# Performance work log

Measured on AMD Instinct MI355X. Metric: run time of the kernel, lower is better.

The kernel has to match this reference:

```python
import jax, jax.numpy as jnp
import numpy as np

RBF_DIM = 16
RBF_DMAX = 10.0
EPS = 1e-8


def _rbf(d):
    # GVP-style radial basis featurization: [..., RBF_DIM]
    mu = jnp.linspace(0.0, RBF_DMAX, RBF_DIM)
    sigma = RBF_DMAX / RBF_DIM
    return jnp.exp(-(((d[..., None] - mu) / sigma) ** 2))


def _norm_no_nan(x):
    return jnp.sqrt(jnp.clip(jnp.sum(x * x, axis=-1), EPS, None))


def setup_inputs() -> dict:
    key = jax.random.key(0)
    ks = jax.random.split(key, 16)
    N, Eu = 100000, 800000
    D_node, D_edge = 128, 64
    n_a, n_e = 16, 5
    s_t = jax.random.normal(ks[0], (N, D_node), jnp.float32)
    x_t = jax.random.normal(ks[1], (N, 3), jnp.float32) * 3.0
    v_t = jax.random.normal(ks[2], (N, 4, 3), jnp.float32)
    e_t = jax.random.normal(ks[3], (2 * Eu, D_edge), jnp.float32)
    dst_lig_x = x_t + jax.random.normal(ks[4], (N, 3), jnp.float32)
    dst_lig_a = jax.random.uniform(ks[5], (N, n_a), jnp.float32)
    dst_lig_e = jax.random.uniform(ks[6], (Eu, n_e), jnp.float32)
    # symmetric edge list: first Eu edges are "upper", second Eu their mirror
    src_u = jax.random.randint(ks[7], (Eu,), 0, N)
    dst_u = jax.random.randint(ks[8], (Eu,), 0, N)
    edge_src = jnp.concatenate([src_u, dst_u]).astype(jnp.int64)
    edge_dst = jnp.concatenate([dst_u, src_u]).astype(jnp.int64)
    # node residual MLP params (in = rbf + one-hot lig_a + s_t)
    din_n = RBF_DIM + n_a + D_node
    W1 = jax.random.normal(ks[9], (din_n, D_node), jnp.float32) / np.sqrt(din_n)
    b1 = jnp.zeros((D_node,), jnp.float32)
    W2 = jax.random.normal(ks[10], (D_node, D_node), jnp.float32) / np.sqrt(D_node)
    b2 = jnp.zeros((D_node,), jnp.float32)
    # edge residual MLP params (in = e_t + lig_e pred + rbf)
    din_e = D_edge + n_e + RBF_DIM
    We = jax.random.normal(ks[11], (din_e, D_edge), jnp.float32) / np.sqrt(din_e)
    be = jnp.zeros((D_edge,), jnp.float32)
    return {"s_t": s_t, "x_t": x_t, "v_t": v_t, "e_t": e_t,
            "dst_lig_x": dst_lig_x, "dst_lig_a": dst_lig_a, "dst_lig_e": dst_lig_e,
            "edge_src": edge_src, "edge_dst": edge_dst,
            "W1": W1, "b1": b1, "W2": W2, "b2": b2, "We": We, "be": be}


def reference(s_t, x_t, v_t, e_t, dst_lig_x, dst_lig_a, dst_lig_e,
              edge_src, edge_dst, W1, b1, W2, b2, We, be):
    # ---- node residual (lig_x generated -> RBF of |x_pred - x_t|; lig_a generated -> pred) ----
    x_diff = dst_lig_x - x_t                      # [N,3]
    dij = _norm_no_nan(x_diff)                    # [N]
    node_in = jnp.concatenate([_rbf(dij), dst_lig_a, s_t], axis=-1)
    h = jax.nn.silu(node_in @ W1 + b1)
    node_res = jax.nn.silu(h @ W2 + b2)
    node_out = s_t + node_res
    # overwrite last vector channel with unit displacement
    v_out = v_t.at[:, -1, :].set(x_diff / dij[:, None])
    # ---- lig_to_lig edge residual on upper edges, mirrored to lower edges ----
    Eu = edge_src.shape[0] // 2
    su, du = edge_src[:Eu], edge_dst[:Eu]
    d_t = _norm_no_nan(x_t[su] - x_t[du])         # current distances
    d_1 = _norm_no_nan(dst_lig_x[su] - dst_lig_x[du])  # predicted distances
    d_input = _rbf(d_1) - _rbf(d_t)               # [Eu, RBF_DIM]
    e_u = e_t[:Eu]
    edge_in = jnp.concatenate([e_u, dst_lig_e, d_input], axis=-1)
    edge_res = jax.nn.silu(edge_in @ We + be)
    feats = e_u + edge_res
    # original scatters feats into both upper-mask and ~upper-mask slots
    e_out = jnp.concatenate([feats, feats], axis=0)
    return node_out, v_out, e_out
```

## Files before the change

### kernel.cpp

```cpp
#include <hip/hip_runtime.h>
#include <math.h>

typedef short bf16x8 __attribute__((ext_vector_type(8)));
typedef float f32x4 __attribute__((ext_vector_type(4)));
typedef float fvec4 __attribute__((ext_vector_type(4)));

#define EBK 128
#define NBK 64

__device__ __forceinline__ float silu_f(float x) {
  return x / (1.0f + __expf(-x));
}
__device__ __forceinline__ unsigned short f2bf(float x) {
  union { float f; unsigned u; } v; v.f = x;
  unsigned r = v.u + 0x7FFFu + ((v.u >> 16) & 1u);
  return (unsigned short)(r >> 16);
}
__device__ __forceinline__ float bf2f(unsigned short h) {
  union { unsigned u; float f; } v; v.u = ((unsigned)h) << 16; return v.f;
}

__global__ __launch_bounds__(256)
void prep_kernel(const float* __restrict__ W1, const float* __restrict__ W2,
                 const float* __restrict__ We, unsigned short* __restrict__ ws)
{
  int i = blockIdx.x * 256 + threadIdx.x;
  if (i < 6144) {
    int col = i / 96, k = i - col * 96;
    float v = (k < 85) ? We[k * 64 + col] : 0.0f;
    ws[i] = f2bf(v);
  }
  int j = i - 6144;
  if (j >= 0 && j < 20480) {
    int col = j / 160, k = j - col * 160;
    ws[6144 + j] = f2bf(W1[k * 128 + col]);
  }
  int l = i - 26624;
  if (l >= 0 && l < 16384) {
    int col = l >> 7, k = l & 127;
    ws[26624 + l] = f2bf(W2[k * 128 + col]);
  }
}

__global__ __launch_bounds__(256, 4)
void node_kernel(const float* __restrict__ s_t,
                 const float* __restrict__ x_t,
                 const float* __restrict__ v_t,
                 const float* __restrict__ dst_lig_x,
                 const float* __restrict__ dst_lig_a,
                 const unsigned short* __restrict__ w1t, const float* __restrict__ b1,
                 const unsigned short* __restrict__ w2t, const float* __restrict__ b2,
                 float* __restrict__ node_out, float* __restrict__ v_out,
                 int N)
{
  __shared__ unsigned short A1[NBK][168];
  __shared__ unsigned short H [NBK][136];
  const int t = threadIdx.x;
  const int row0 = blockIdx.x * NBK;
  const int w = t >> 6, lane = t & 63;

  #pragma unroll
  for (int p = 0; p < 8; ++p) {
    int i = p * 256 + t;
    int row = i >> 5, q = i & 31;
    if (row0 + row < N) {
      const fvec4 v = __builtin_nontemporal_load(
          reinterpret_cast<const fvec4*>(&s_t[(size_t)(row0 + row) * 128 + q * 4]));
      uint2 pk;
      pk.x = f2bf(v.x) | ((unsigned)f2bf(v.y) << 16);
      pk.y = f2bf(v.z) | ((unsigned)f2bf(v.w) << 16);
      *reinterpret_cast<uint2*>(&A1[row][32 + q * 4]) = pk;
    }
  }
  #pragma unroll
  for (int p = 0; p < 4; ++p) {
    int i = p * 256 + t;
    int el = i >> 4, m = i & 15;
    int row = row0 + el;
    if (row < N) {
      float dx = dst_lig_x[row*3+0] - x_t[row*3+0];
      float dy = dst_lig_x[row*3+1] - x_t[row*3+1];
      float dz = dst_lig_x[row*3+2] - x_t[row*3+2];
      float dij = sqrtf(fmaxf(dx*dx + dy*dy + dz*dz, 1e-8f));
      float tt = (dij - 0.66666667f * (float)m) * 1.6f;
      A1[el][m]      = f2bf(__expf(-tt * tt));
      A1[el][16 + m] = f2bf(dst_lig_a[(size_t)row * 16 + m]);
      if (m < 12) {
        float val;
        if (m < 9)       val = v_t[(size_t)row * 12 + m];
        else if (m == 9) val = dx / dij;
        else if (m == 10)val = dy / dij;
        else             val = dz / dij;
        __builtin_nontemporal_store(val, &v_out[(size_t)row * 12 + m]);
      }
    }
  }
  __syncthreads();

  const int mb = (w & 1) * 32;
  const int nb = (w >> 1) * 64;

  f32x4 acc[2][4] = {};
  #pragma unroll 1
  for (int ks = 0; ks < 5; ++ks) {
    const int ko = ks * 32 + ((lane >> 4) << 3);
    bf16x8 af[2], bfr[4];
    #pragma unroll
    for (int m = 0; m < 2; ++m)
      af[m] = *reinterpret_cast<const bf16x8*>(&A1[mb + m*16 + (lane & 15)][ko]);
    #pragma unroll
    for (int n = 0; n < 4; ++n)
      bfr[n] = *reinterpret_cast<const bf16x8*>(&w1t[(size_t)(nb + n*16 + (lane & 15)) * 160 + ko]);
    #pragma unroll
    for (int m = 0; m < 2; ++m)
      #pragma unroll
      for (int n = 0; n < 4; ++n)
        acc[m][n] = __builtin_amdgcn_mfma_f32_16x16x32_bf16(af[m], bfr[n], acc[m][n], 0, 0, 0);
  }
  #pragma unroll
  for (int n = 0; n < 4; ++n) {
    float bb = b1[nb + n*16 + (lane & 15)];
    #pragma unroll
    for (int m = 0; m < 2; ++m) {
      int r0 = mb + m*16 + ((lane >> 4) << 2);
      int c  = nb + n*16 + (lane & 15);
      #pragma unroll
      for (int r = 0; r < 4; ++r)
        H[r0 + r][c] = f2bf(silu_f(acc[m][n][r] + bb));
    }
  }
  __syncthreads();

  f32x4 acc2[2][4] = {};
  #pragma unroll 1
  for (int ks = 0; ks < 4; ++ks) {
    const int ko = ks * 32 + ((lane >> 4) << 3);
    bf16x8 af[2], bfr[4];
    #pragma unroll
    for (int m = 0; m < 2; ++m)
      af[m] = *reinterpret_cast<const bf16x8*>(&H[mb + m*16 + (lane & 15)][ko]);
    #pragma unroll
    for (int n = 0; n < 4; ++n)
      bfr[n] = *reinterpret_cast<const bf16x8*>(&w2t[(size_t)(nb + n*16 + (lane & 15)) * 128 + ko]);
    #pragma unroll
    for (int m = 0; m < 2; ++m)
      #pragma unroll
      for (int n = 0; n < 4; ++n)
        acc2[m][n] = __builtin_amdgcn_mfma_f32_16x16x32_bf16(af[m], bfr[n], acc2[m][n], 0, 0, 0);
  }
  #pragma unroll
  for (int n = 0; n < 4; ++n) {
    float bb = b2[nb + n*16 + (lane & 15)];
    #pragma unroll
    for (int m = 0; m < 2; ++m) {
      int r0 = mb + m*16 + ((lane >> 4) << 2);
      int c  = nb + n*16 + (lane & 15);
      #pragma unroll
      for (int r = 0; r < 4; ++r) {
        int row = row0 + r0 + r;
        if (row < N) {
          float o = bf2f(A1[r0 + r][32 + c]) + silu_f(acc2[m][n][r] + bb);
          __builtin_nontemporal_store(o, &node_out[(size_t)row * 128 + c]);
        }
      }
    }
  }
}

__global__ __launch_bounds__(256, 6)
void edge_kernel(const float* __restrict__ e_t,
                 const float* __restrict__ x_t,
                 const float* __restrict__ dst_lig_x,
                 const float* __restrict__ dst_lig_e,
                 const int* __restrict__ edge_src,
                 const int* __restrict__ edge_dst,
                 const unsigned short* __restrict__ wet, const float* __restrict__ be,
                 float* __restrict__ e_out0, float* __restrict__ e_out1,
                 int Eu)
{
  __shared__ unsigned short T[EBK][36];
  const int t = threadIdx.x;
  const int e0 = blockIdx.x * EBK;
  const int w = t >> 6, lane = t & 63;

  {
    const int el = t >> 1, which = t & 1;
    const int e = e0 + el;
    float dcur = 0.0f;
    if (e < Eu) {
      int su = edge_src[e], du = edge_dst[e];
      const float* base = which ? dst_lig_x : x_t;
      float u0 = base[su*3+0] - base[du*3+0];
      float u1 = base[su*3+1] - base[du*3+1];
      float u2 = base[su*3+2] - base[du*3+2];
      dcur = sqrtf(fmaxf(u0*u0 + u1*u1 + u2*u2, 1e-8f));
    }
    float doth = __shfl_xor(dcur, 1);
    float dt_ = which ? doth : dcur;
    float d1_ = which ? dcur : doth;
    if (e < Eu) {
      #pragma unroll
      for (int q = 0; q < 8; ++q) {
        int m = which * 8 + q;
        float mu = 0.66666667f * (float)m;
        float a1 = (d1_ - mu) * 1.6f, a2 = (dt_ - mu) * 1.6f;
        T[el][5 + m] = f2bf(__expf(-a1*a1) - __expf(-a2*a2));
      }
    }
  }
  #pragma unroll
  for (int q = 0; q < 3; ++q) {
    int i = q * 256 + t;
    if (i < EBK * 5) {
      int el = i / 5, c = i - el * 5;
      if (e0 + el < Eu) T[el][c] = f2bf(dst_lig_e[(size_t)(e0 + el) * 5 + c]);
    }
  }
  #pragma unroll
  for (int q = 0; q < 6; ++q) {
    int i = q * 256 + t;
    if (i < EBK * 11) { int el = i / 11, c = i - el * 11; T[el][21 + c] = 0; }
  }
  __syncthreads();

  const int mb = w * 32;
  const int lr = lane & 15;
  const int koff = (lane >> 4) << 3;

  f32x4 acc[2][4] = {};
  #pragma unroll 1
  for (int ks = 0; ks < 2; ++ks) {
    bf16x8 af[2], bfr[4];
    #pragma unroll
    for (int m = 0; m < 2; ++m) {
      int row = e0 + mb + m*16 + lr;
      if (row >= Eu) row = Eu - 1;
      const float* ap = &e_t[(size_t)row * 64 + ks * 32 + koff];
      const fvec4 lo = *reinterpret_cast<const fvec4*>(ap);
      const fvec4 hi = *reinterpret_cast<const fvec4*>(ap + 4);
      union { bf16x8 v; unsigned u[4]; } pk;
      pk.u[0] = f2bf(lo.x) | ((unsigned)f2bf(lo.y) << 16);
      pk.u[1] = f2bf(lo.z) | ((unsigned)f2bf(lo.w) << 16);
      pk.u[2] = f2bf(hi.x) | ((unsigned)f2bf(hi.y) << 16);
      pk.u[3] = f2bf(hi.z) | ((unsigned)f2bf(hi.w) << 16);
      af[m] = pk.v;
    }
    #pragma unroll
    for (int n = 0; n < 4; ++n)
      bfr[n] = *reinterpret_cast<const bf16x8*>(&wet[(size_t)(n*16 + lr) * 96 + ks * 32 + koff]);
    #pragma unroll
    for (int m = 0; m < 2; ++m)
      #pragma unroll
      for (int n = 0; n < 4; ++n)
        acc[m][n] = __builtin_amdgcn_mfma_f32_16x16x32_bf16(af[m], bfr[n], acc[m][n], 0, 0, 0);
  }
  {
    bf16x8 af[2], bfr[4];
    #pragma unroll
    for (int m = 0; m < 2; ++m)
      af[m] = *reinterpret_cast<const bf16x8*>(&T[mb + m*16 + lr][koff]);
    #pragma unroll
    for (int n = 0; n < 4; ++n)
      bfr[n] = *reinterpret_cast<const bf16x8*>(&wet[(size_t)(n*16 + lr) * 96 + 64 + koff]);
    #pragma unroll
    for (int m = 0; m < 2; ++m)
      #pragma unroll
      for (int n = 0; n < 4; ++n)
        acc[m][n] = __builtin_amdgcn_mfma_f32_16x16x32_bf16(af[m], bfr[n], acc[m][n], 0, 0, 0);
  }

  #pragma unroll
  for (int n = 0; n < 4; ++n) {
    float bb = be[n*16 + lr];
    #pragma unroll
    for (int m = 0; m < 2; ++m) {
      int r0 = mb + m*16 + ((lane >> 4) << 2);
      int c  = n*16 + lr;
      #pragma unroll
      for (int r = 0; r < 4; ++r) {
        size_t eidx = (size_t)e0 + r0 + r;
        if ((int)eidx < Eu) {
          float feat = e_t[eidx * 64 + c] + silu_f(acc[m][n][r] + bb);
          __builtin_nontemporal_store(feat, &e_out0[eidx * 64 + c]);
          __builtin_nontemporal_store(feat, &e_out1[eidx * 64 + c]);
        }
      }
    }
  }
}

extern "C" void kernel_launch(void* const* d_in, const int* in_sizes, int n_in,
                              void* d_out, int out_size, void* d_ws, size_t ws_size,
                              hipStream_t stream) {
  const float* s_t       = (const float*)d_in[0];
  const float* x_t       = (const float*)d_in[1];
  const float* v_t       = (const float*)d_in[2];
  const float* e_t       = (const float*)d_in[3];
  const float* dst_lig_x = (const float*)d_in[4];
  const float* dst_lig_a = (const float*)d_in[5];
  const float* dst_lig_e = (const float*)d_in[6];
  const int*   edge_src  = (const int*)d_in[7];
  const int*   edge_dst  = (const int*)d_in[8];
  const float* W1        = (const float*)d_in[9];
  const float* b1        = (const float*)d_in[10];
  const float* W2        = (const float*)d_in[11];
  const float* b2        = (const float*)d_in[12];
  const float* We        = (const float*)d_in[13];
  const float* be        = (const float*)d_in[14];

  const int N  = in_sizes[0] / 128;
  const int Eu = in_sizes[3] / 128;

  float* out      = (float*)d_out;
  float* node_out = out;
  float* v_out    = out + (size_t)N * 128;
  float* e_out0   = v_out + (size_t)N * 12;
  float* e_out1   = e_out0 + (size_t)Eu * 64;

  unsigned short* wsp = (unsigned short*)d_ws;
  unsigned short* wet = wsp;
  unsigned short* w1t = wsp + 6144;
  unsigned short* w2t = wsp + 26624;

  prep_kernel<<<168, 256, 0, stream>>>(W1, W2, We, wsp);

  edge_kernel<<<(Eu + EBK - 1) / EBK, 256, 0, stream>>>(
      e_t, x_t, dst_lig_x, dst_lig_e, edge_src, edge_dst, wet, be,
      e_out0, e_out1, Eu);

  node_kernel<<<(N + NBK - 1) / NBK, 256, 0, stream>>>(
      s_t, x_t, v_t, dst_lig_x, dst_lig_a, w1t, b1, w2t, b2,
      node_out, v_out, N);
}
```

Before: 246.9 us.

## Use 512-thread edge blocks with early e_t loads and one M-tile per wave

The edge kernel now launches 512 threads per block, so each of 8 waves handles one 16-row M tile instead of two. The e_t A-fragment loads are issued before the RBF/LDS staging phase so their latency overlaps that work. The residual e_t reads are also batched into registers ahead of the epilogue, and the fp32-to-bf16 conversion becomes truncation instead of round-to-nearest-even. Truncation slightly changes numerical accuracy, and launch_bounds(512,6) may constrain registers.

```diff
diff --git a/kernel.cpp b/kernel.cpp
--- a/kernel.cpp
+++ b/kernel.cpp
@@ -18,6 +18,10 @@
 }
 __device__ __forceinline__ float bf2f(unsigned short h) {
   union { unsigned u; float f; } v; v.u = ((unsigned)h) << 16; return v.f;
+}
+__device__ __forceinline__ unsigned pack_trunc(float lo, float hi) {
+  union { float f; unsigned u; } a, b; a.f = lo; b.f = hi;
+  return (b.u & 0xFFFF0000u) | (a.u >> 16);
 }
 
 __global__ __launch_bounds__(256)
@@ -167,7 +171,7 @@
   }
 }
 
-__global__ __launch_bounds__(256, 6)
+__global__ __launch_bounds__(512, 6)
 void edge_kernel(const float* __restrict__ e_t,
                  const float* __restrict__ x_t,
                  const float* __restrict__ dst_lig_x,
@@ -182,8 +186,20 @@
   const int t = threadIdx.x;
   const int e0 = blockIdx.x * EBK;
   const int w = t >> 6, lane = t & 63;
-
-  {
+  const int lr = lane & 15;
+  const int koff = (lane >> 4) << 3;
+  const int mb = w * 16;
+
+  int arow = e0 + mb + lr;
+  if (arow >= Eu) arow = Eu - 1;
+  const fvec4* ap = reinterpret_cast<const fvec4*>(&e_t[(size_t)arow * 64]);
+  const int fi = koff >> 2;
+  fvec4 a00 = ap[fi];
+  fvec4 a01 = ap[fi + 1];
+  fvec4 a10 = ap[8 + fi];
+  fvec4 a11 = ap[8 + fi + 1];
+
+  if (t < 256) {
     const int el = t >> 1, which = t & 1;
     const int e = e0 + el;
     float dcur = 0.0f;
@@ -209,81 +225,81 @@
     }
   }
   #pragma unroll
-  for (int q = 0; q < 3; ++q) {
-    int i = q * 256 + t;
+  for (int q = 0; q < 2; ++q) {
+    int i = q * 512 + t;
     if (i < EBK * 5) {
       int el = i / 5, c = i - el * 5;
       if (e0 + el < Eu) T[el][c] = f2bf(dst_lig_e[(size_t)(e0 + el) * 5 + c]);
     }
   }
   #pragma unroll
-  for (int q = 0; q < 6; ++q) {
-    int i = q * 256 + t;
+  for (int q = 0; q < 3; ++q) {
+    int i = q * 512 + t;
     if (i < EBK * 11) { int el = i / 11, c = i - el * 11; T[el][21 + c] = 0; }
   }
   __syncthreads();
 
-  const int mb = w * 32;
-  const int lr = lane & 15;
-  const int koff = (lane >> 4) << 3;
-
-  f32x4 acc[2][4] = {};
-  #pragma unroll 1
-  for (int ks = 0; ks < 2; ++ks) {
-    bf16x8 af[2], bfr[4];
-    #pragma unroll
-    for (int m = 0; m < 2; ++m) {
-      int row = e0 + mb + m*16 + lr;
-      if (row >= Eu) row = Eu - 1;
-      const float* ap = &e_t[(size_t)row * 64 + ks * 32 + koff];
-      const fvec4 lo = *reinterpret_cast<const fvec4*>(ap);
-      const fvec4 hi = *reinterpret_cast<const fvec4*>(ap + 4);
-      union { bf16x8 v; unsigned u[4]; } pk;
-      pk.u[0] = f2bf(lo.x) | ((unsigned)f2bf(lo.y) << 16);
-      pk.u[1] = f2bf(lo.z) | ((unsigned)f2bf(lo.w) << 16);
-      pk.u[2] = f2bf(hi.x) | ((unsigned)f2bf(hi.y) << 16);
-      pk.u[3] = f2bf(hi.z) | ((unsigned)f2bf(hi.w) << 16);
-      af[m] = pk.v;
-    }
-    #pragma unroll
-    for (int n = 0; n < 4; ++n)
-      bfr[n] = *reinterpret_cast<const bf16x8*>(&wet[(size_t)(n*16 + lr) * 96 + ks * 32 + koff]);
-    #pragma unroll
-    for (int m = 0; m < 2; ++m)
-      #pragma unroll
-      for (int n = 0; n < 4; ++n)
-        acc[m][n] = __builtin_amdgcn_mfma_f32_16x16x32_bf16(af[m], bfr[n], acc[m][n], 0, 0, 0);
-  }
+  union { bf16x8 v; unsigned u[4]; } af0, af1, af2;
+  af0.u[0] = pack_trunc(a00.x, a00.y);
+  af0.u[1] = pack_trunc(a00.z, a00.w);
+  af0.u[2] = pack_trunc(a01.x, a01.y);
+  af0.u[3] = pack_trunc(a01.z, a01.w);
+  af1.u[0] = pack_trunc(a10.x, a10.y);
+  af1.u[1] = pack_trunc(a10.z, a10.w);
+  af1.u[2] = pack_trunc(a11.x, a11.y);
+  af1.u[3] = pack_trunc(a11.z, a11.w);
+  af2.v = *reinterpret_cast<const bf16x8*>(&T[mb + lr][koff]);
+
+  f32x4 acc[4] = {};
   {
-    bf16x8 af[2], bfr[4];
-    #pragma unroll
-    for (int m = 0; m < 2; ++m)
-      af[m] = *reinterpret_cast<const bf16x8*>(&T[mb + m*16 + lr][koff]);
-    #pragma unroll
-    for (int n = 0; n < 4; ++n)
-      bfr[n] = *reinterpret_cast<const bf16x8*>(&wet[(size_t)(n*16 + lr) * 96 + 64 + koff]);
-    #pragma unroll
-    for (int m = 0; m < 2; ++m)
-      #pragma unroll
-      for (int n = 0; n < 4; ++n)
-        acc[m][n] = __builtin_amdgcn_mfma_f32_16x16x32_bf16(af[m], bfr[n], acc[m][n], 0, 0, 0);
-  }
-
+    bf16x8 b0, b1_, b2_, b3;
+    b0 = *reinterpret_cast<const bf16x8*>(&wet[(size_t)(0*16 + lr) * 96 + 0*32 + koff]);
+    b1_= *reinterpret_cast<const bf16x8*>(&wet[(size_t)(1*16 + lr) * 96 + 0*32 + koff]);
+    b2_= *reinterpret_cast<const bf16x8*>(&wet[(size_t)(2*16 + lr) * 96 + 0*32 + koff]);
+    b3 = *reinterpret_cast<const bf16x8*>(&wet[(size_t)(3*16 + lr) * 96 + 0*32 + koff]);
+    acc[0] = __builtin_amdgcn_mfma_f32_16x16x32_bf16(af0.v, b0, acc[0], 0, 0, 0);
+    acc[1] = __builtin_amdgcn_mfma_f32_16x16x32_bf16(af0.v, b1_, acc[1], 0, 0, 0);
+    acc[2] = __builtin_amdgcn_mfma_f32_16x16x32_bf16(af0.v, b2_, acc[2], 0, 0, 0);
+    acc[3] = __builtin_amdgcn_mfma_f32_16x16x32_bf16(af0.v, b3, acc[3], 0, 0, 0);
+    b0 = *reinterpret_cast<const bf16x8*>(&wet[(size_t)(0*16 + lr) * 96 + 1*32 + koff]);
+    b1_= *reinterpret_cast<const bf16x8*>(&wet[(size_t)(1*16 + lr) * 96 + 1*32 + koff]);
+    b2_= *reinterpret_cast<const bf16x8*>(&wet[(size_t)(2*16 + lr) * 96 + 1*32 + koff]);
+    b3 = *reinterpret_cast<const bf16x8*>(&wet[(size_t)(3*16 + lr) * 96 + 1*32 + koff]);
+    acc[0] = __builtin_amdgcn_mfma_f32_16x16x32_bf16(af1.v, b0, acc[0], 0, 0, 0);
+    acc[1] = __builtin_amdgcn_mfma_f32_16x16x32_bf16(af1.v, b1_, acc[1], 0, 0, 0);
+    acc[2] = __builtin_amdgcn_mfma_f32_16x16x32_bf16(af1.v, b2_, acc[2], 0, 0, 0);
+    acc[3] = __builtin_amdgcn_mfma_f32_16x16x32_bf16(af1.v, b3, acc[3], 0, 0, 0);
+    b0 = *reinterpret_cast<const bf16x8*>(&wet[(size_t)(0*16 + lr) * 96 + 64 + koff]);
+    b1_= *reinterpret_cast<const bf16x8*>(&wet[(size_t)(1*16 + lr) * 96 + 64 + koff]);
+    b2_= *reinterpret_cast<const bf16x8*>(&wet[(size_t)(2*16 + lr) * 96 + 64 + koff]);
+    b3 = *reinterpret_cast<const bf16x8*>(&wet[(size_t)(3*16 + lr) * 96 + 64 + koff]);
+    acc[0] = __builtin_amdgcn_mfma_f32_16x16x32_bf16(af2.v, b0, acc[0], 0, 0, 0);
+    acc[1] = __builtin_amdgcn_mfma_f32_16x16x32_bf16(af2.v, b1_, acc[1], 0, 0, 0);
+    acc[2] = __builtin_amdgcn_mfma_f32_16x16x32_bf16(af2.v, b2_, acc[2], 0, 0, 0);
+    acc[3] = __builtin_amdgcn_mfma_f32_16x16x32_bf16(af2.v, b3, acc[3], 0, 0, 0);
+  }
+
+  const int r0 = mb + ((lane >> 4) << 2);
+  float res[4][4];
+  #pragma unroll
+  for (int n = 0; n < 4; ++n)
+    #pragma unroll
+    for (int r = 0; r < 4; ++r) {
+      size_t eidx = (size_t)e0 + r0 + r;
+      if ((int)eidx >= Eu) eidx = Eu - 1;
+      res[n][r] = e_t[eidx * 64 + n*16 + lr];
+    }
   #pragma unroll
   for (int n = 0; n < 4; ++n) {
     float bb = be[n*16 + lr];
-    #pragma unroll
-    for (int m = 0; m < 2; ++m) {
-      int r0 = mb + m*16 + ((lane >> 4) << 2);
-      int c  = n*16 + lr;
-      #pragma unroll
-      for (int r = 0; r < 4; ++r) {
-        size_t eidx = (size_t)e0 + r0 + r;
-        if ((int)eidx < Eu) {
-          float feat = e_t[eidx * 64 + c] + silu_f(acc[m][n][r] + bb);
-          __builtin_nontemporal_store(feat, &e_out0[eidx * 64 + c]);
-          __builtin_nontemporal_store(feat, &e_out1[eidx * 64 + c]);
-        }
+    int c = n*16 + lr;
+    #pragma unroll
+    for (int r = 0; r < 4; ++r) {
+      size_t eidx = (size_t)e0 + r0 + r;
+      if ((int)eidx < Eu) {
+        float feat = res[n][r] + silu_f(acc[n][r] + bb);
+        __builtin_nontemporal_store(feat, &e_out0[eidx * 64 + c]);
+        __builtin_nontemporal_store(feat, &e_out1[eidx * 64 + c]);
       }
     }
   }
@@ -324,7 +340,7 @@
 
   prep_kernel<<<168, 256, 0, stream>>>(W1, W2, We, wsp);
 
-  edge_kernel<<<(Eu + EBK - 1) / EBK, 256, 0, stream>>>(
+  edge_kernel<<<(Eu + EBK - 1) / EBK, 512, 0, stream>>>(
       e_t, x_t, dst_lig_x, dst_lig_e, edge_src, edge_dst, wet, be,
       e_out0, e_out1, Eu);
 
```

Result: slower. 262.0 us (+6.1%).

## Fuse node and edge kernels into one interleaved launch with shared LDS union

Applied to the files above, without the earlier changes.

Merges the separate edge and node kernels into one launch in which every fifth block does node work and the rest do edge work, so the two kinds of blocks overlap on the device instead of running back to back. Node and edge tiles share LDS through a union, and the hidden-layer buffer H now reuses the A1 space, with an extra barrier added to make that safe. The node residual now rereads s_t from global memory instead of the bf16 copy in LDS, which also changes rounding of the residual. The risks are that node blocks now run under the edge kernel's launch bounds (fewer registers), and that the branch makes the block mix uneven.

```diff
diff --git a/kernel.cpp b/kernel.cpp
--- a/kernel.cpp
+++ b/kernel.cpp
@@ -42,247 +42,257 @@
   }
 }
 
-__global__ __launch_bounds__(256, 4)
-void node_kernel(const float* __restrict__ s_t,
-                 const float* __restrict__ x_t,
-                 const float* __restrict__ v_t,
-                 const float* __restrict__ dst_lig_x,
-                 const float* __restrict__ dst_lig_a,
-                 const unsigned short* __restrict__ w1t, const float* __restrict__ b1,
-                 const unsigned short* __restrict__ w2t, const float* __restrict__ b2,
-                 float* __restrict__ node_out, float* __restrict__ v_out,
-                 int N)
+struct NodeSmem { unsigned short A1[NBK][168]; };
+struct EdgeSmem { unsigned short T[EBK][36]; };
+union FusedSmem { NodeSmem n; EdgeSmem e; };
+
+__global__ __launch_bounds__(256, 6)
+void fused_kernel(const float* __restrict__ s_t,
+                  const float* __restrict__ x_t,
+                  const float* __restrict__ v_t,
+                  const float* __restrict__ e_t,
+                  const float* __restrict__ dst_lig_x,
+                  const float* __restrict__ dst_lig_a,
+                  const float* __restrict__ dst_lig_e,
+                  const int* __restrict__ edge_src,
+                  const int* __restrict__ edge_dst,
+                  const unsigned short* __restrict__ wsw,
+                  const float* __restrict__ b1, const float* __restrict__ b2,
+                  const float* __restrict__ be,
+                  float* __restrict__ node_out, float* __restrict__ v_out,
+                  float* __restrict__ e_out0, float* __restrict__ e_out1,
+                  int N, int Eu, int nNodeBlk, int nEdgeBlk)
 {
-  __shared__ unsigned short A1[NBK][168];
-  __shared__ unsigned short H [NBK][136];
+  __shared__ FusedSmem sm;
+  const int bid = blockIdx.x;
   const int t = threadIdx.x;
-  const int row0 = blockIdx.x * NBK;
   const int w = t >> 6, lane = t & 63;
-
-  #pragma unroll
-  for (int p = 0; p < 8; ++p) {
-    int i = p * 256 + t;
-    int row = i >> 5, q = i & 31;
-    if (row0 + row < N) {
-      const fvec4 v = __builtin_nontemporal_load(
-          reinterpret_cast<const fvec4*>(&s_t[(size_t)(row0 + row) * 128 + q * 4]));
-      uint2 pk;
-      pk.x = f2bf(v.x) | ((unsigned)f2bf(v.y) << 16);
-      pk.y = f2bf(v.z) | ((unsigned)f2bf(v.w) << 16);
-      *reinterpret_cast<uint2*>(&A1[row][32 + q * 4]) = pk;
-    }
-  }
-  #pragma unroll
-  for (int p = 0; p < 4; ++p) {
-    int i = p * 256 + t;
-    int el = i >> 4, m = i & 15;
-    int row = row0 + el;
-    if (row < N) {
-      float dx = dst_lig_x[row*3+0] - x_t[row*3+0];
-      float dy = dst_lig_x[row*3+1] - x_t[row*3+1];
-      float dz = dst_lig_x[row*3+2] - x_t[row*3+2];
-      float dij = sqrtf(fmaxf(dx*dx + dy*dy + dz*dz, 1e-8f));
-      float tt = (dij - 0.66666667f * (float)m) * 1.6f;
-      A1[el][m]      = f2bf(__expf(-tt * tt));
-      A1[el][16 + m] = f2bf(dst_lig_a[(size_t)row * 16 + m]);
-      if (m < 12) {
-        float val;
-        if (m < 9)       val = v_t[(size_t)row * 12 + m];
-        else if (m == 9) val = dx / dij;
-        else if (m == 10)val = dy / dij;
-        else             val = dz / dij;
-        __builtin_nontemporal_store(val, &v_out[(size_t)row * 12 + m]);
-      }
-    }
-  }
-  __syncthreads();
-
-  const int mb = (w & 1) * 32;
-  const int nb = (w >> 1) * 64;
-
-  f32x4 acc[2][4] = {};
-  #pragma unroll 1
-  for (int ks = 0; ks < 5; ++ks) {
-    const int ko = ks * 32 + ((lane >> 4) << 3);
-    bf16x8 af[2], bfr[4];
-    #pragma unroll
-    for (int m = 0; m < 2; ++m)
-      af[m] = *reinterpret_cast<const bf16x8*>(&A1[mb + m*16 + (lane & 15)][ko]);
-    #pragma unroll
-    for (int n = 0; n < 4; ++n)
-      bfr[n] = *reinterpret_cast<const bf16x8*>(&w1t[(size_t)(nb + n*16 + (lane & 15)) * 160 + ko]);
-    #pragma unroll
-    for (int m = 0; m < 2; ++m)
-      #pragma unroll
-      for (int n = 0; n < 4; ++n)
-        acc[m][n] = __builtin_amdgcn_mfma_f32_16x16x32_bf16(af[m], bfr[n], acc[m][n], 0, 0, 0);
-  }
-  #pragma unroll
-  for (int n = 0; n < 4; ++n) {
-    float bb = b1[nb + n*16 + (lane & 15)];
-    #pragma unroll
-    for (int m = 0; m < 2; ++m) {
-      int r0 = mb + m*16 + ((lane >> 4) << 2);
-      int c  = nb + n*16 + (lane & 15);
-      #pragma unroll
-      for (int r = 0; r < 4; ++r)
-        H[r0 + r][c] = f2bf(silu_f(acc[m][n][r] + bb));
-    }
-  }
-  __syncthreads();
-
-  f32x4 acc2[2][4] = {};
-  #pragma unroll 1
-  for (int ks = 0; ks < 4; ++ks) {
-    const int ko = ks * 32 + ((lane >> 4) << 3);
-    bf16x8 af[2], bfr[4];
-    #pragma unroll
-    for (int m = 0; m < 2; ++m)
-      af[m] = *reinterpret_cast<const bf16x8*>(&H[mb + m*16 + (lane & 15)][ko]);
-    #pragma unroll
-    for (int n = 0; n < 4; ++n)
-      bfr[n] = *reinterpret_cast<const bf16x8*>(&w2t[(size_t)(nb + n*16 + (lane & 15)) * 128 + ko]);
-    #pragma unroll
-    for (int m = 0; m < 2; ++m)
-      #pragma unroll
-      for (int n = 0; n < 4; ++n)
-        acc2[m][n] = __builtin_amdgcn_mfma_f32_16x16x32_bf16(af[m], bfr[n], acc2[m][n], 0, 0, 0);
-  }
-  #pragma unroll
-  for (int n = 0; n < 4; ++n) {
-    float bb = b2[nb + n*16 + (lane & 15)];
-    #pragma unroll
-    for (int m = 0; m < 2; ++m) {
-      int r0 = mb + m*16 + ((lane >> 4) << 2);
-      int c  = nb + n*16 + (lane & 15);
-      #pragma unroll
-      for (int r = 0; r < 4; ++r) {
-        int row = row0 + r0 + r;
-        if (row < N) {
-          float o = bf2f(A1[r0 + r][32 + c]) + silu_f(acc2[m][n][r] + bb);
-          __builtin_nontemporal_store(o, &node_out[(size_t)row * 128 + c]);
-        }
-      }
-    }
-  }
-}
-
-__global__ __launch_bounds__(256, 6)
-void edge_kernel(const float* __restrict__ e_t,
-                 const float* __restrict__ x_t,
-                 const float* __restrict__ dst_lig_x,
-                 const float* __restrict__ dst_lig_e,
-                 const int* __restrict__ edge_src,
-                 const int* __restrict__ edge_dst,
-                 const unsigned short* __restrict__ wet, const float* __restrict__ be,
-                 float* __restrict__ e_out0, float* __restrict__ e_out1,
-                 int Eu)
-{
-  __shared__ unsigned short T[EBK][36];
-  const int t = threadIdx.x;
-  const int e0 = blockIdx.x * EBK;
-  const int w = t >> 6, lane = t & 63;
-
-  {
-    const int el = t >> 1, which = t & 1;
-    const int e = e0 + el;
-    float dcur = 0.0f;
-    if (e < Eu) {
-      int su = edge_src[e], du = edge_dst[e];
-      const float* base = which ? dst_lig_x : x_t;
-      float u0 = base[su*3+0] - base[du*3+0];
-      float u1 = base[su*3+1] - base[du*3+1];
-      float u2 = base[su*3+2] - base[du*3+2];
-      dcur = sqrtf(fmaxf(u0*u0 + u1*u1 + u2*u2, 1e-8f));
-    }
-    float doth = __shfl_xor(dcur, 1);
-    float dt_ = which ? doth : dcur;
-    float d1_ = which ? dcur : doth;
-    if (e < Eu) {
-      #pragma unroll
-      for (int q = 0; q < 8; ++q) {
-        int m = which * 8 + q;
-        float mu = 0.66666667f * (float)m;
-        float a1 = (d1_ - mu) * 1.6f, a2 = (dt_ - mu) * 1.6f;
-        T[el][5 + m] = f2bf(__expf(-a1*a1) - __expf(-a2*a2));
-      }
-    }
-  }
-  #pragma unroll
-  for (int q = 0; q < 3; ++q) {
-    int i = q * 256 + t;
-    if (i < EBK * 5) {
-      int el = i / 5, c = i - el * 5;
-      if (e0 + el < Eu) T[el][c] = f2bf(dst_lig_e[(size_t)(e0 + el) * 5 + c]);
-    }
-  }
-  #pragma unroll
-  for (int q = 0; q < 6; ++q) {
-    int i = q * 256 + t;
-    if (i < EBK * 11) { int el = i / 11, c = i - el * 11; T[el][21 + c] = 0; }
-  }
-  __syncthreads();
-
-  const int mb = w * 32;
   const int lr = lane & 15;
   const int koff = (lane >> 4) << 3;
 
-  f32x4 acc[2][4] = {};
-  #pragma unroll 1
-  for (int ks = 0; ks < 2; ++ks) {
-    bf16x8 af[2], bfr[4];
-    #pragma unroll
-    for (int m = 0; m < 2; ++m) {
-      int row = e0 + mb + m*16 + lr;
-      if (row >= Eu) row = Eu - 1;
-      const float* ap = &e_t[(size_t)row * 64 + ks * 32 + koff];
-      const fvec4 lo = *reinterpret_cast<const fvec4*>(ap);
-      const fvec4 hi = *reinterpret_cast<const fvec4*>(ap + 4);
-      union { bf16x8 v; unsigned u[4]; } pk;
-      pk.u[0] = f2bf(lo.x) | ((unsigned)f2bf(lo.y) << 16);
-      pk.u[1] = f2bf(lo.z) | ((unsigned)f2bf(lo.w) << 16);
-      pk.u[2] = f2bf(hi.x) | ((unsigned)f2bf(hi.y) << 16);
-      pk.u[3] = f2bf(hi.z) | ((unsigned)f2bf(hi.w) << 16);
-      af[m] = pk.v;
-    }
-    #pragma unroll
-    for (int n = 0; n < 4; ++n)
-      bfr[n] = *reinterpret_cast<const bf16x8*>(&wet[(size_t)(n*16 + lr) * 96 + ks * 32 + koff]);
-    #pragma unroll
-    for (int m = 0; m < 2; ++m)
+  if (bid % 5 == 4) {
+    const int nb = bid / 5;
+    if (nb >= nNodeBlk) return;
+    const int row0 = nb * NBK;
+    const unsigned short* w1t = wsw + 6144;
+    const unsigned short* w2t = wsw + 26624;
+    auto& A1 = sm.n.A1;
+    unsigned short* Hp = &sm.n.A1[0][0];
+
+    #pragma unroll
+    for (int p = 0; p < 8; ++p) {
+      int i = p * 256 + t;
+      int row = i >> 5, q = i & 31;
+      if (row0 + row < N) {
+        const fvec4 v = __builtin_nontemporal_load(
+            reinterpret_cast<const fvec4*>(&s_t[(size_t)(row0 + row) * 128 + q * 4]));
+        uint2 pk;
+        pk.x = f2bf(v.x) | ((unsigned)f2bf(v.y) << 16);
+        pk.y = f2bf(v.z) | ((unsigned)f2bf(v.w) << 16);
+        *reinterpret_cast<uint2*>(&A1[row][32 + q * 4]) = pk;
+      }
+    }
+    #pragma unroll
+    for (int p = 0; p < 4; ++p) {
+      int i = p * 256 + t;
+      int el = i >> 4, m = i & 15;
+      int row = row0 + el;
+      if (row < N) {
+        float dx = dst_lig_x[row*3+0] - x_t[row*3+0];
+        float dy = dst_lig_x[row*3+1] - x_t[row*3+1];
+        float dz = dst_lig_x[row*3+2] - x_t[row*3+2];
+        float dij = sqrtf(fmaxf(dx*dx + dy*dy + dz*dz, 1e-8f));
+        float tt = (dij - 0.66666667f * (float)m) * 1.6f;
+        A1[el][m]      = f2bf(__expf(-tt * tt));
+        A1[el][16 + m] = f2bf(dst_lig_a[(size_t)row * 16 + m]);
+        if (m < 12) {
+          float val;
+          if (m < 9)       val = v_t[(size_t)row * 12 + m];
+          else if (m == 9) val = dx / dij;
+          else if (m == 10)val = dy / dij;
+          else             val = dz / dij;
+          __builtin_nontemporal_store(val, &v_out[(size_t)row * 12 + m]);
+        }
+      }
+    }
+    __syncthreads();
+
+    const int mb = (w & 1) * 32;
+    const int nb2 = (w >> 1) * 64;
+
+    f32x4 acc[2][4] = {};
+    #pragma unroll 1
+    for (int ks = 0; ks < 5; ++ks) {
+      const int ko = ks * 32 + koff;
+      bf16x8 af[2], bfr[4];
+      #pragma unroll
+      for (int m = 0; m < 2; ++m)
+        af[m] = *reinterpret_cast<const bf16x8*>(&A1[mb + m*16 + lr][ko]);
       #pragma unroll
       for (int n = 0; n < 4; ++n)
-        acc[m][n] = __builtin_amdgcn_mfma_f32_16x16x32_bf16(af[m], bfr[n], acc[m][n], 0, 0, 0);
-  }
-  {
-    bf16x8 af[2], bfr[4];
-    #pragma unroll
-    for (int m = 0; m < 2; ++m)
-      af[m] = *reinterpret_cast<const bf16x8*>(&T[mb + m*16 + lr][koff]);
-    #pragma unroll
-    for (int n = 0; n < 4; ++n)
-      bfr[n] = *reinterpret_cast<const bf16x8*>(&wet[(size_t)(n*16 + lr) * 96 + 64 + koff]);
-    #pragma unroll
-    for (int m = 0; m < 2; ++m)
+        bfr[n] = *reinterpret_cast<const bf16x8*>(&w1t[(size_t)(nb2 + n*16 + lr) * 160 + ko]);
+      #pragma unroll
+      for (int m = 0; m < 2; ++m)
+        #pragma unroll
+        for (int n = 0; n < 4; ++n)
+          acc[m][n] = __builtin_amdgcn_mfma_f32_16x16x32_bf16(af[m], bfr[n], acc[m][n], 0, 0, 0);
+    }
+    __syncthreads();
+
+    #pragma unroll
+    for (int n = 0; n < 4; ++n) {
+      float bb = b1[nb2 + n*16 + lr];
+      #pragma unroll
+      for (int m = 0; m < 2; ++m) {
+        int r0 = mb + m*16 + ((lane >> 4) << 2);
+        int c  = nb2 + n*16 + lr;
+        #pragma unroll
+        for (int r = 0; r < 4; ++r)
+          Hp[(size_t)(r0 + r) * 136 + c] = f2bf(silu_f(acc[m][n][r] + bb));
+      }
+    }
+    __syncthreads();
+
+    f32x4 acc2[2][4] = {};
+    #pragma unroll 1
+    for (int ks = 0; ks < 4; ++ks) {
+      const int ko = ks * 32 + koff;
+      bf16x8 af[2], bfr[4];
+      #pragma unroll
+      for (int m = 0; m < 2; ++m)
+        af[m] = *reinterpret_cast<const bf16x8*>(&Hp[(size_t)(mb + m*16 + lr) * 136 + ko]);
       #pragma unroll
       for (int n = 0; n < 4; ++n)
-        acc[m][n] = __builtin_amdgcn_mfma_f32_16x16x32_bf16(af[m], bfr[n], acc[m][n], 0, 0, 0);
-  }
-
-  #pragma unroll
-  for (int n = 0; n < 4; ++n) {
-    float bb = be[n*16 + lr];
-    #pragma unroll
-    for (int m = 0; m < 2; ++m) {
-      int r0 = mb + m*16 + ((lane >> 4) << 2);
-      int c  = n*16 + lr;
-      #pragma unroll
-      for (int r = 0; r < 4; ++r) {
-        size_t eidx = (size_t)e0 + r0 + r;
-        if ((int)eidx < Eu) {
-          float feat = e_t[eidx * 64 + c] + silu_f(acc[m][n][r] + bb);
-          __builtin_nontemporal_store(feat, &e_out0[eidx * 64 + c]);
-          __builtin_nontemporal_store(feat, &e_out1[eidx * 64 + c]);
+        bfr[n] = *reinterpret_cast<const bf16x8*>(&w2t[(size_t)(nb2 + n*16 + lr) * 128 + ko]);
+      #pragma unroll
+      for (int m = 0; m < 2; ++m)
+        #pragma unroll
+        for (int n = 0; n < 4; ++n)
+          acc2[m][n] = __builtin_amdgcn_mfma_f32_16x16x32_bf16(af[m], bfr[n], acc2[m][n], 0, 0, 0);
+    }
+    #pragma unroll
+    for (int n = 0; n < 4; ++n) {
+      float bb = b2[nb2 + n*16 + lr];
+      #pragma unroll
+      for (int m = 0; m < 2; ++m) {
+        int r0 = mb + m*16 + ((lane >> 4) << 2);
+        int c  = nb2 + n*16 + lr;
+        #pragma unroll
+        for (int r = 0; r < 4; ++r) {
+          int row = row0 + r0 + r;
+          if (row < N) {
+            float o = s_t[(size_t)row * 128 + c] + silu_f(acc2[m][n][r] + bb);
+            __builtin_nontemporal_store(o, &node_out[(size_t)row * 128 + c]);
+          }
+        }
+      }
+    }
+  } else {
+    const int eb = bid - (bid + 1) / 5;
+    if (eb >= nEdgeBlk) return;
+    const int e0 = eb * EBK;
+    const unsigned short* wet = wsw;
+    auto& T = sm.e.T;
+
+    {
+      const int el = t >> 1, which = t & 1;
+      const int e = e0 + el;
+      float dcur = 0.0f;
+      if (e < Eu) {
+        int su = edge_src[e], du = edge_dst[e];
+        const float* base = which ? dst_lig_x : x_t;
+        float u0 = base[su*3+0] - base[du*3+0];
+        float u1 = base[su*3+1] - base[du*3+1];
+        float u2 = base[su*3+2] - base[du*3+2];
+        dcur = sqrtf(fmaxf(u0*u0 + u1*u1 + u2*u2, 1e-8f));
+      }
+      float doth = __shfl_xor(dcur, 1);
+      float dt_ = which ? doth : dcur;
+      float d1_ = which ? dcur : doth;
+      if (e < Eu) {
+        #pragma unroll
+        for (int q = 0; q < 8; ++q) {
+          int m = which * 8 + q;
+          float mu = 0.66666667f * (float)m;
+          float a1 = (d1_ - mu) * 1.6f, a2 = (dt_ - mu) * 1.6f;
+          T[el][5 + m] = f2bf(__expf(-a1*a1) - __expf(-a2*a2));
+        }
+      }
+    }
+    #pragma unroll
+    for (int q = 0; q < 3; ++q) {
+      int i = q * 256 + t;
+      if (i < EBK * 5) {
+        int el = i / 5, c = i - el * 5;
+        if (e0 + el < Eu) T[el][c] = f2bf(dst_lig_e[(size_t)(e0 + el) * 5 + c]);
+      }
+    }
+    #pragma unroll
+    for (int q = 0; q < 6; ++q) {
+      int i = q * 256 + t;
+      if (i < EBK * 11) { int el = i / 11, c = i - el * 11; T[el][21 + c] = 0; }
+    }
+    __syncthreads();
+
+    const int mb = w * 32;
+
+    f32x4 acc[2][4] = {};
+    #pragma unroll 1
+    for (int ks = 0; ks < 2; ++ks) {
+      bf16x8 af[2], bfr[4];
+      #pragma unroll
+      for (int m = 0; m < 2; ++m) {
+        int row = e0 + mb + m*16 + lr;
+        if (row >= Eu) row = Eu - 1;
+        const float* ap = &e_t[(size_t)row * 64 + ks * 32 + koff];
+        const fvec4 lo = *reinterpret_cast<const fvec4*>(ap);
+        const fvec4 hi = *reinterpret_cast<const fvec4*>(ap + 4);
+        union { bf16x8 v; unsigned u[4]; } pk;
+        pk.u[0] = f2bf(lo.x) | ((unsigned)f2bf(lo.y) << 16);
+        pk.u[1] = f2bf(lo.z) | ((unsigned)f2bf(lo.w) << 16);
+        pk.u[2] = f2bf(hi.x) | ((unsigned)f2bf(hi.y) << 16);
+        pk.u[3] = f2bf(hi.z) | ((unsigned)f2bf(hi.w) << 16);
+        af[m] = pk.v;
+      }
+      #pragma unroll
+      for (int n = 0; n < 4; ++n)
+        bfr[n] = *reinterpret_cast<const bf16x8*>(&wet[(size_t)(n*16 + lr) * 96 + ks * 32 + koff]);
+      #pragma unroll
+      for (int m = 0; m < 2; ++m)
+        #pragma unroll
+        for (int n = 0; n < 4; ++n)
+          acc[m][n] = __builtin_amdgcn_mfma_f32_16x16x32_bf16(af[m], bfr[n], acc[m][n], 0, 0, 0);
+    }
+    {
+      bf16x8 af[2], bfr[4];
+      #pragma unroll
+      for (int m = 0; m < 2; ++m)
+        af[m] = *reinterpret_cast<const bf16x8*>(&T[mb + m*16 + lr][koff]);
+      #pragma unroll
+      for (int n = 0; n < 4; ++n)
+        bfr[n] = *reinterpret_cast<const bf16x8*>(&wet[(size_t)(n*16 + lr) * 96 + 64 + koff]);
+      #pragma unroll
+      for (int m = 0; m < 2; ++m)
+        #pragma unroll
+        for (int n = 0; n < 4; ++n)
+          acc[m][n] = __builtin_amdgcn_mfma_f32_16x16x32_bf16(af[m], bfr[n], acc[m][n], 0, 0, 0);
+    }
+
+    #pragma unroll
+    for (int n = 0; n < 4; ++n) {
+      float bb = be[n*16 + lr];
+      #pragma unroll
+      for (int m = 0; m < 2; ++m) {
+        int r0 = mb + m*16 + ((lane >> 4) << 2);
+        int c  = n*16 + lr;
+        #pragma unroll
+        for (int r = 0; r < 4; ++r) {
+          size_t eidx = (size_t)e0 + r0 + r;
+          if ((int)eidx < Eu) {
+            float feat = e_t[eidx * 64 + c] + silu_f(acc[m][n][r] + bb);
+            __builtin_nontemporal_store(feat, &e_out0[eidx * 64 + c]);
+            __builtin_nontemporal_store(feat, &e_out1[eidx * 64 + c]);
+          }
         }
       }
     }
@@ -318,17 +328,15 @@
   float* e_out1   = e_out0 + (size_t)Eu * 64;
 
   unsigned short* wsp = (unsigned short*)d_ws;
-  unsigned short* wet = wsp;
-  unsigned short* w1t = wsp + 6144;
-  unsigned short* w2t = wsp + 26624;
+
+  const int NBLK = (N + NBK - 1) / NBK;
+  const int EBLK = (Eu + EBK - 1) / EBK;
+  int grid = 5 * NBLK;
+  if (grid - NBLK < EBLK) grid = 5 * NBLK + (EBLK - 4 * NBLK) + ((EBLK - 4 * NBLK) / 4 + 1);
 
   prep_kernel<<<168, 256, 0, stream>>>(W1, W2, We, wsp);
 
-  edge_kernel<<<(Eu + EBK - 1) / EBK, 256, 0, stream>>>(
-      e_t, x_t, dst_lig_x, dst_lig_e, edge_src, edge_dst, wet, be,
-      e_out0, e_out1, Eu);
-
-  node_kernel<<<(N + NBK - 1) / NBK, 256, 0, stream>>>(
-      s_t, x_t, v_t, dst_lig_x, dst_lig_a, w1t, b1, w2t, b2,
-      node_out, v_out, N);
-}
+  fused_kernel<<<grid, 256, 0, stream>>>(
+      s_t, x_t, v_t, e_t, dst_lig_x, dst_lig_a, dst_lig_e, edge_src, edge_dst,
+      wsp, b1, b2, be, node_out, v_out, e_out0, e_out1, N, Eu, NBLK, EBLK);
+}
```

After: 323.6 us. 1.31x slower.
